# Performance work log

Measured on AMD Instinct MI355X. Metric: run time of the kernel, lower is better.

The kernel has to match this reference:

```python
import jax, jax.numpy as jnp
import numpy as np

B, N = 256, 65536

def setup_inputs() -> dict:
    key = jax.random.key(0)
    k1, k2 = jax.random.split(key)
    I1 = jax.random.normal(k1, (B, N, 2), dtype=jnp.float32)
    I2 = jax.random.normal(k2, (B, N, 2), dtype=jnp.float32)
    return {"I1": I1, "I2": I2}

def reference(I1, I2):
    # Complex multiply, elementwise over (B, N)
    real = I1[..., 0] * I2[..., 0] - I1[..., 1] * I2[..., 1]  # (B, N)
    imag = I1[..., 1] * I2[..., 0] + I1[..., 0] * I2[..., 1]  # (B, N)
    # Original torch code cats (1,2,N) -> flat order [reals..., imags...]
    # then .view(-1,2), pairing consecutive elements of that flat sequence.
    flat = jnp.concatenate([real, imag], axis=-1)  # (B, 2N)
    return flat.reshape(I1.shape[0], -1, 2)        # (B, N, 2)
```

## Files before the change

kernel.cpp:

```cpp
#include <hip/hip_runtime.h>
#include <hip/hip_bf16.h>


#define N_COMPLEX 65536
#define ROW_F4    (2 * N_COMPLEX / 4)
#define IMAG_OFF_F4 (N_COMPLEX / 4)

__global__ __launch_bounds__(256) void cmul_kernel(
        const float4* __restrict__ a,
        const float4* __restrict__ b,
        float4* __restrict__ out) {
    const unsigned int t = blockIdx.x * blockDim.x + threadIdx.x;
    const unsigned int row = t >> 14;
    const unsigned int n4  = t & 16383;

    const size_t in4 = (size_t)t * 2;
    const float4 a0 = a[in4];
    const float4 a1 = a[in4 + 1];
    const float4 b0 = b[in4];
    const float4 b1 = b[in4 + 1];

    float4 re, im;
    re.x = a0.x * b0.x - a0.y * b0.y;
    im.x = a0.y * b0.x + a0.x * b0.y;
    re.y = a0.z * b0.z - a0.w * b0.w;
    im.y = a0.w * b0.z + a0.z * b0.w;
    re.z = a1.x * b1.x - a1.y * b1.y;
    im.z = a1.y * b1.x + a1.x * b1.y;
    re.w = a1.z * b1.z - a1.w * b1.w;
    im.w = a1.w * b1.z + a1.z * b1.w;

    const size_t base = (size_t)row * ROW_F4 + n4;
    out[base]               = re;
    out[base + IMAG_OFF_F4] = im;
}

extern "C" void kernel_launch(void* const* d_in, const int* in_sizes, int n_in,
                              void* d_out, int out_size, void* d_ws, size_t ws_size,
                              hipStream_t stream) {
    const float4* a = (const float4*)d_in[0];
    const float4* b = (const float4*)d_in[1];
    float4* out = (float4*)d_out;

    const int threads_total = out_size / 8;
    const int block = 256;
    const int grid = threads_total / block;
    cmul_kernel<<<grid, block, 0, stream>>>(a, b, out);
}
```

Baseline: 303.9 us.

## Use persistent grid-stride loop with unrolled loads and nontemporal stores

Replaces the one-thread-per-element launch with a fixed grid of 2048 blocks that loops over the data with a stride. Each iteration batches four independent float4 loads per input to raise memory-level parallelism. Outputs are written as float2 with nontemporal stores to avoid polluting cache. The narrower store width may reduce per-instruction efficiency, and the grid size is hard-coded to the problem shape.

Result: slower. 323.0 us (+6.3%).

```diff
diff --git a/kernel.cpp b/kernel.cpp
--- a/kernel.cpp
+++ b/kernel.cpp
@@ -1,49 +1,55 @@
 #include <hip/hip_runtime.h>
-#include <hip/hip_bf16.h>
 
 
-#define N_COMPLEX 65536
-#define ROW_F4    (2 * N_COMPLEX / 4)
-#define IMAG_OFF_F4 (N_COMPLEX / 4)
+#define N_COMPLEX   65536
+#define ROW_F4_IN   (N_COMPLEX / 2)
+#define IMAG_OFF_F2 (N_COMPLEX / 2)
+#define BLOCK       256
+#define GRID        2048
+#define STRIDE      (BLOCK * GRID)
+#define TOTAL_F4    (256 * (N_COMPLEX / 2))
+#define ITERS       (TOTAL_F4 / STRIDE)
+#define UNROLL      4
 
-__global__ __launch_bounds__(256) void cmul_kernel(
-        const float4* __restrict__ a,
-        const float4* __restrict__ b,
-        float4* __restrict__ out) {
-    const unsigned int t = blockIdx.x * blockDim.x + threadIdx.x;
-    const unsigned int row = t >> 14;
-    const unsigned int n4  = t & 16383;
+typedef float f32x2 __attribute__((ext_vector_type(2)));
+typedef float f32x4 __attribute__((ext_vector_type(4)));
 
-    const size_t in4 = (size_t)t * 2;
-    const float4 a0 = a[in4];
-    const float4 a1 = a[in4 + 1];
-    const float4 b0 = b[in4];
-    const float4 b1 = b[in4 + 1];
-
-    float4 re, im;
-    re.x = a0.x * b0.x - a0.y * b0.y;
-    im.x = a0.y * b0.x + a0.x * b0.y;
-    re.y = a0.z * b0.z - a0.w * b0.w;
-    im.y = a0.w * b0.z + a0.z * b0.w;
-    re.z = a1.x * b1.x - a1.y * b1.y;
-    im.z = a1.y * b1.x + a1.x * b1.y;
-    re.w = a1.z * b1.z - a1.w * b1.w;
-    im.w = a1.w * b1.z + a1.z * b1.w;
-
-    const size_t base = (size_t)row * ROW_F4 + n4;
-    out[base]               = re;
-    out[base + IMAG_OFF_F4] = im;
+__global__ __launch_bounds__(BLOCK) void cmul_kernel(
+        const f32x4* __restrict__ a,
+        const f32x4* __restrict__ b,
+        f32x2* __restrict__ out) {
+    unsigned idx = blockIdx.x * BLOCK + threadIdx.x;
+    #pragma unroll 1
+    for (int o = 0; o < ITERS / UNROLL; ++o) {
+        f32x4 va[UNROLL], vb[UNROLL];
+        unsigned id[UNROLL];
+        #pragma unroll
+        for (int i = 0; i < UNROLL; ++i) {
+            id[i] = idx + (unsigned)i * STRIDE;
+            va[i] = a[id[i]];
+            vb[i] = b[id[i]];
+        }
+        #pragma unroll
+        for (int i = 0; i < UNROLL; ++i) {
+            f32x2 re, im;
+            re.x = va[i].x * vb[i].x - va[i].y * vb[i].y;
+            im.x = va[i].y * vb[i].x + va[i].x * vb[i].y;
+            re.y = va[i].z * vb[i].z - va[i].w * vb[i].w;
+            im.y = va[i].w * vb[i].z + va[i].z * vb[i].w;
+            const unsigned r2 = ((id[i] & ~(unsigned)(ROW_F4_IN - 1)) << 1)
+                              | (id[i] & (unsigned)(ROW_F4_IN - 1));
+            __builtin_nontemporal_store(re, &out[r2]);
+            __builtin_nontemporal_store(im, &out[r2 + IMAG_OFF_F2]);
+        }
+        idx += UNROLL * STRIDE;
+    }
 }
 
 extern "C" void kernel_launch(void* const* d_in, const int* in_sizes, int n_in,
                               void* d_out, int out_size, void* d_ws, size_t ws_size,
                               hipStream_t stream) {
-    const float4* a = (const float4*)d_in[0];
-    const float4* b = (const float4*)d_in[1];
-    float4* out = (float4*)d_out;
-
-    const int threads_total = out_size / 8;
-    const int block = 256;
-    const int grid = threads_total / block;
-    cmul_kernel<<<grid, block, 0, stream>>>(a, b, out);
+    (void)in_sizes; (void)n_in; (void)d_ws; (void)ws_size; (void)out_size;
+    cmul_kernel<<<GRID, BLOCK, 0, stream>>>((const f32x4*)d_in[0],
+                                            (const f32x4*)d_in[1],
+                                            (f32x2*)d_out);
 }
```
